# Optimization experiments

Measured on AMD Instinct MI355X. Metric: run time of the kernel, lower is better.

Reference implementation:

```python
import jax, jax.numpy as jnp
import numpy as np

B, S, D, H, O = 32, 2048, 512, 512, 512


def setup_inputs() -> dict:
    key = jax.random.key(0)
    ks = jax.random.split(key, 10)
    def w(k, shape, fan_in):
        return (jax.random.uniform(k, shape, dtype=jnp.float32) * 2.0 - 1.0) / np.float32(np.sqrt(fan_in))
    return {
        "x": jax.random.normal(ks[0], (B, S, D), dtype=jnp.float32),
        "timespans": jax.random.uniform(ks[1], (B, S, 1), dtype=jnp.float32),
        "Wx_lstm": w(ks[2], (D, 4 * H), D),
        "Wh_lstm": w(ks[3], (H, 4 * H), H),
        "b_lstm": jnp.zeros((4 * H,), dtype=jnp.float32),
        "Wx_ode": w(ks[4], (D, H), D),
        "Wh_ode": w(ks[5], (H, H), H),
        "b_ode": jnp.zeros((H,), dtype=jnp.float32),
        "Wfc": w(ks[6], (H, O), H),
        "bfc": jnp.zeros((O,), dtype=jnp.float32),
    }


def reference(x, timespans, Wx_lstm, Wh_lstm, b_lstm, Wx_ode, Wh_ode, b_ode, Wfc, bfc):
    b, s, d = x.shape
    h_dim = Wh_ode.shape[0]
    # Precompute input projections for all timesteps (hoisted out of the scan).
    xz_lstm = jnp.einsum('bsd,dk->bsk', x, Wx_lstm) + b_lstm   # (B,S,4H)
    xz_ode = jnp.einsum('bsd,dh->bsh', x, Wx_ode) + b_ode      # (B,S,H)
    ts = timespans[..., 0]                                      # (B,S), matches ts.squeeze()

    def step(carry, inp):
        h, c = carry
        zl, zo, t = inp                      # (B,4H), (B,H), (B,)
        # LSTM memory update (mixed-memory part)
        z = zl + h @ Wh_lstm
        i, f, g, o = jnp.split(z, 4, axis=-1)
        c_new = jax.nn.sigmoid(f) * c + jax.nn.sigmoid(i) * jnp.tanh(g)
        h_mem = jax.nn.sigmoid(o) * jnp.tanh(c_new)
        # Heun (RK2) ODE step: dh/dt = tanh(Wx x + Wh h + b)
        def f_ode(hh):
            return jnp.tanh(zo + hh @ Wh_ode)
        tcol = t[:, None]
        k1 = f_ode(h_mem)
        k2 = f_ode(h_mem + tcol * k1)
        h_new = h_mem + 0.5 * tcol * (k1 + k2)
        return (h_new, c_new), h_new

    carry0 = (jnp.zeros((b, h_dim), x.dtype), jnp.zeros((b, h_dim), x.dtype))
    xs = (jnp.swapaxes(xz_lstm, 0, 1), jnp.swapaxes(xz_ode, 0, 1), ts.T)
    (h_last, c_last), hs = jax.lax.scan(step, carry0, xs)       # hs: (S,B,H)
    outputs = jnp.einsum('sbh,ho->sbo', hs, Wfc) + bfc
    outputs = jnp.swapaxes(outputs, 0, 1)                       # (B,S,O)
    return outputs, h_last, c_last
```

## Files before the change

kernel.cpp:

```cpp
#include <hip/hip_runtime.h>

typedef unsigned short u16;
typedef unsigned int u32;
typedef unsigned long long u64;
typedef __attribute__((ext_vector_type(4))) float f32x4;
typedef __attribute__((ext_vector_type(8))) short bf16x8;
typedef __attribute__((ext_vector_type(4))) u16 u16x4;
typedef __attribute__((ext_vector_type(8))) u16 u16x8;
typedef __attribute__((ext_vector_type(4))) u32 u32x4;

#define AGENT_SCOPE __HIP_MEMORY_SCOPE_AGENT

__device__ __forceinline__ u64 lda64(const u64* p) {
  return __hip_atomic_load((u64*)p, __ATOMIC_RELAXED, AGENT_SCOPE);
}
__device__ __forceinline__ int loadai(const int* p) {
  return __hip_atomic_load((int*)p, __ATOMIC_RELAXED, AGENT_SCOPE);
}
__device__ __forceinline__ void sta32(u32* p, u32 v) {
  __hip_atomic_store(p, v, __ATOMIC_RELAXED, AGENT_SCOPE);
}

__device__ __forceinline__ u16 f2bf(float f) {
  u32 u = __builtin_bit_cast(u32, f);
  u = (u + 0x7FFFu + ((u >> 16) & 1u)) >> 16;
  return (u16)u;
}
__device__ __forceinline__ float b2f(u16 h) {
  return __builtin_bit_cast(float, ((u32)h) << 16);
}
__device__ __forceinline__ float sigf(float x) { return 1.0f / (1.0f + __expf(-x)); }
__device__ __forceinline__ float tanh_(float x) { return 2.0f / (1.0f + __expf(-2.0f * x)) - 1.0f; }

__global__ __launch_bounds__(256) void cvt_bf16_vec(
    const float* __restrict__ in, u16* __restrict__ out, int n4)
{
  int i = blockIdx.x * blockDim.x + threadIdx.x;
  const int stride = gridDim.x * blockDim.x;
  for (; i < n4; i += stride) {
    f32x4 v = ((const f32x4*)in)[i];
    u16x4 o;
    #pragma unroll
    for (int e = 0; e < 4; ++e) o[e] = f2bf(v[e]);
    ((u16x4*)out)[i] = o;
  }
}

__global__ __launch_bounds__(256) void transpose_f32_bf16(
    const float* __restrict__ in, u16* __restrict__ out, int R, int C)
{
  __shared__ float t[32][33];
  const int tx = threadIdx.x & 31, ty = threadIdx.x >> 5;
  const int bx = blockIdx.x * 32, by = blockIdx.y * 32;
  #pragma unroll
  for (int i = 0; i < 4; ++i)
    t[ty + i * 8][tx] = in[(long)(by + ty + i * 8) * C + bx + tx];
  __syncthreads();
  #pragma unroll
  for (int i = 0; i < 4; ++i)
    out[(long)(bx + ty + i * 8) * R + by + tx] = f2bf(t[tx][ty + i * 8]);
}

template <bool BF16_OUT>
__global__ __launch_bounds__(256, 2) void gemm_bt(
    const u16* __restrict__ A, const u16* __restrict__ Bt,
    const float* __restrict__ bias, void* __restrict__ Cv,
    int M, int N, int K)
{
  __shared__ u16 As[128 * 64];
  __shared__ u16 Bs[128 * 64];
  const int tid = threadIdx.x;
  const int lane = tid & 63;
  const int wv = tid >> 6;
  const int wm = wv >> 1, wn = wv & 1;
  const long row0 = (long)blockIdx.x * 128;
  const long col0 = (long)blockIdx.y * 128;
  const int lr8 = lane >> 3, lc8 = lane & 7;
  const int fr = lane & 15, fk = (lane >> 4) * 8;
  f32x4 acc[4][4] = {};

  for (int kt = 0; kt < K; kt += 64) {
    __syncthreads();
    #pragma unroll
    for (int ch = 0; ch < 4; ++ch) {
      const int r = wv * 32 + ch * 8;
      const u16* gA = A + (row0 + r + lr8) * (long)K + kt + lc8 * 8;
      __builtin_amdgcn_global_load_lds(
          (const __attribute__((address_space(1))) u32*)gA,
          (__attribute__((address_space(3))) u32*)&As[r * 64], 16, 0, 0);
      const u16* gB = Bt + (col0 + r + lr8) * (long)K + kt + lc8 * 8;
      __builtin_amdgcn_global_load_lds(
          (const __attribute__((address_space(1))) u32*)gB,
          (__attribute__((address_space(3))) u32*)&Bs[r * 64], 16, 0, 0);
    }
    __syncthreads();
    #pragma unroll
    for (int kk = 0; kk < 2; ++kk) {
      bf16x8 af[4], bfv[4];
      #pragma unroll
      for (int m = 0; m < 4; ++m)
        af[m] = *(const bf16x8*)&As[(wm * 64 + m * 16 + fr) * 64 + kk * 32 + fk];
      #pragma unroll
      for (int n = 0; n < 4; ++n)
        bfv[n] = *(const bf16x8*)&Bs[(wn * 64 + n * 16 + fr) * 64 + kk * 32 + fk];
      #pragma unroll
      for (int m = 0; m < 4; ++m)
        #pragma unroll
        for (int n = 0; n < 4; ++n)
          acc[m][n] = __builtin_amdgcn_mfma_f32_16x16x32_bf16(af[m], bfv[n], acc[m][n], 0, 0, 0);
    }
  }

  const int orow = (lane >> 4) * 4, ocol = lane & 15;
  #pragma unroll
  for (int m = 0; m < 4; ++m) {
    #pragma unroll
    for (int n = 0; n < 4; ++n) {
      const long cb = col0 + wn * 64 + n * 16 + ocol;
      const float bv = bias[cb];
      #pragma unroll
      for (int r = 0; r < 4; ++r) {
        const long rr = row0 + wm * 64 + m * 16 + orow + r;
        const float v = acc[m][n][r] + bv;
        if (BF16_OUT) ((u16*)Cv)[rr * (long)N + cb] = f2bf(v);
        else          ((float*)Cv)[rr * (long)N + cb] = v;
      }
    }
  }
}

#define SS 2048
#define FAROFF 16384

__device__ __forceinline__ bool ge4(u32x4 v, u32 t) {
  return ((v[0] >> 16) >= t) & ((v[1] >> 16) >= t) &
         ((v[2] >> 16) >= t) & ((v[3] >> 16) >= t);
}
__device__ __forceinline__ bool ge2(u64 w, u32 t) {
  return ((((u32)(w >> 16)) & 0xffffu) >= t) & (((u32)(w >> 48)) >= t);
}

__device__ __forceinline__ void ld8_sc0(const u32* p, u32x4& a, u32x4& b) {
  asm volatile("global_load_dwordx4 %0, %2, off sc0\n\t"
               "global_load_dwordx4 %1, %3, off sc0\n\t"
               "s_waitcnt vmcnt(0)"
               : "=&v"(a), "=&v"(b) : "v"(p), "v"(p + 4));
}
__device__ __forceinline__ void ld8_sc1(const u32* p, u32x4& a, u32x4& b) {
  asm volatile("global_load_dwordx4 %0, %2, off sc1\n\t"
               "global_load_dwordx4 %1, %3, off sc1\n\t"
               "s_waitcnt vmcnt(0)"
               : "=&v"(a), "=&v"(b) : "v"(p), "v"(p + 4));
}

__device__ __forceinline__ void pollfar(const u32* pf, u32 tag, u32x4& a, u32x4& b) {
  const u64* q = (const u64*)pf;
  u64 w0 = lda64(q), w1 = lda64(q + 1), w2 = lda64(q + 2), w3 = lda64(q + 3);
  int tries = 0;
  while (!(ge2(w0, tag) & ge2(w1, tag) & ge2(w2, tag) & ge2(w3, tag))) {
    if (++tries > 2) __builtin_amdgcn_s_sleep(1);
    w0 = lda64(q); w1 = lda64(q + 1); w2 = lda64(q + 2); w3 = lda64(q + 3);
  }
  a[0] = (u32)w0; a[1] = (u32)(w0 >> 32); a[2] = (u32)w1; a[3] = (u32)(w1 >> 32);
  b[0] = (u32)w2; b[1] = (u32)(w2 >> 32); b[2] = (u32)w3; b[3] = (u32)(w3 >> 32);
}

__device__ __forceinline__ void poll8(const u32* pn, u32 tag, int lvl, int* lvlsh,
                                      u32x4& a, u32x4& b) {
  if (lvl == 0) {
    int tries = 0;
    for (;;) {
      ld8_sc0(pn, a, b);
      if (ge4(a, tag) && ge4(b, tag)) return;
      if (++tries > 8000) { *lvlsh = 1; lvl = 1; break; }
      if (tries > 32) __builtin_amdgcn_s_sleep(1);
    }
  }
  if (lvl == 1) {
    int tries = 0;
    for (;;) {
      ld8_sc1(pn, a, b);
      if (ge4(a, tag) && ge4(b, tag)) return;
      if (++tries > 8000) { *lvlsh = 2; break; }
      if (tries > 32) __builtin_amdgcn_s_sleep(1);
    }
  }
  pollfar(pn + FAROFF, tag, a, b);
}

__device__ __forceinline__ void stdual(u32* pn, u32 word, bool far_grp) {
  sta32(pn + FAROFF, word);
  if (!far_grp)
    asm volatile("global_store_dword %0, %1, off sc1" :: "v"(pn), "v"(word) : "memory");
}

__global__ __launch_bounds__(256, 1) void scan_kernel(
    const u16* __restrict__ XZL, const float* __restrict__ XZO,
    const float* __restrict__ TS,
    const u16* __restrict__ WhlT, const u16* __restrict__ WhoT,
    u32* Ht, u32* HMt, u32* Ut,
    u16* __restrict__ HS,
    float* __restrict__ out_h, float* __restrict__ out_c,
    int* chk)
{
  const int tid = threadIdx.x;
  const int lane = tid & 63;
  const int wv = tid >> 6;
  const int fr = lane & 15;
  const int hi = lane >> 4;

  __shared__ u16 whl_l[4][16][512];
  __shared__ u16 who_l[16][512];
  __shared__ u16 stage_l[4][512];
  __shared__ u16 xcl[256];
  __shared__ int lvl_sh;

  if (tid == 0) {
    u32 xcc;
    asm volatile("s_getreg_b32 %0, hwreg(HW_REG_XCC_ID)" : "=s"(xcc));
    sta32((u32*)&chk[blockIdx.x], (xcc & 7u) + 1u);
    lvl_sh = 0;
  }
  {
    int v;
    do { v = loadai(&chk[tid]); } while (v == 0);
    xcl[tid] = (u16)(v - 1);
  }
  __syncthreads();

  int g, w;
  bool far_grp;
  {
    int cnt[8] = {0, 0, 0, 0, 0, 0, 0, 0};
    const int my = (int)xcl[blockIdx.x];
    int rank = 0;
    for (int bi = 0; bi < 256; ++bi) {
      const int e = (int)xcl[bi];
      ++cnt[e];
      rank += (e == my && bi < (int)blockIdx.x) ? 1 : 0;
    }
    bool ok = true;
    #pragma unroll
    for (int e = 0; e < 8; ++e) ok = ok && (cnt[e] == 32);
    if (ok) { g = my; w = rank; far_grp = false; }
    else    { g = (int)(blockIdx.x & 7); w = (int)(blockIdx.x >> 3); far_grp = true; }
  }
  const int j0 = w * 16;
  const int b = g * 4 + wv;

  {
    const int g4 = wv;
    #pragma unroll
    for (int ks = 0; ks < 16; ++ks)
      *(u16x8*)&whl_l[g4][ks][lane * 8] =
        *(const u16x8*)&WhlT[(size_t)(g4 * 512 + j0 + fr) * 512 + ks * 32 + hi * 8];
    for (int ks = wv; ks < 16; ks += 4)
      *(u16x8*)&who_l[ks][lane * 8] =
        *(const u16x8*)&WhoT[(size_t)(j0 + fr) * 512 + ks * 32 + hi * 8];
  }
  __syncthreads();

  u32* const Hb  = Ht  + g * 2048 + wv * 512;
  u32* const HMb = HMt + g * 2048 + wv * 512;
  u32* const Ub  = Ut  + g * 2048 + wv * 512;

  float zb_c[4], zo_c, t_c;
  {
    const u16* p = XZL + ((size_t)b * SS + 0) * 2048 + j0 + fr;
    zb_c[0] = b2f(p[0]); zb_c[1] = b2f(p[512]);
    zb_c[2] = b2f(p[1024]); zb_c[3] = b2f(p[1536]);
    zo_c = XZO[((size_t)b * SS + 0) * 512 + j0 + fr];
    t_c  = TS[(size_t)b * SS + 0];
  }

  float c_r = 0.0f;
  u32x4 pa, pb;

  for (int s = 0; s < SS; ++s) {
    const u32 tagv = (u32)(s + 1);
    int lvl = far_grp ? 2 : *(volatile int*)&lvl_sh;

    if (s == 0) {
      u16x8 z8 = {0, 0, 0, 0, 0, 0, 0, 0};
      *(u16x8*)&stage_l[wv][lane * 8] = z8;
    } else {
      poll8(Hb + lane * 8, (u32)s, lvl, &lvl_sh, pa, pb);
      u16x8 hv;
      #pragma unroll
      for (int i = 0; i < 4; ++i) {
        hv[i] = (u16)(pa[i] & 0xffffu);
        hv[4 + i] = (u16)(pb[i] & 0xffffu);
      }
      *(u16x8*)&stage_l[wv][lane * 8] = hv;
    }

    f32x4 az0 = {}, az1 = {}, az2 = {}, az3 = {};
    #pragma unroll
    for (int ks = 0; ks < 16; ++ks) {
      bf16x8 af = *(const bf16x8*)&stage_l[wv][ks * 32 + hi * 8];
      az0 = __builtin_amdgcn_mfma_f32_16x16x32_bf16(af, *(const bf16x8*)&whl_l[0][ks][lane * 8], az0, 0, 0, 0);
      az1 = __builtin_amdgcn_mfma_f32_16x16x32_bf16(af, *(const bf16x8*)&whl_l[1][ks][lane * 8], az1, 0, 0, 0);
      az2 = __builtin_amdgcn_mfma_f32_16x16x32_bf16(af, *(const bf16x8*)&whl_l[2][ks][lane * 8], az2, 0, 0, 0);
      az3 = __builtin_amdgcn_mfma_f32_16x16x32_bf16(af, *(const bf16x8*)&whl_l[3][ks][lane * 8], az3, 0, 0, 0);
    }

    const float zi = az0[0] + zb_c[0];
    const float zf = az1[0] + zb_c[1];
    const float zg = az2[0] + zb_c[2];
    const float zo = az3[0] + zb_c[3];
    const float cn = sigf(zf) * c_r + sigf(zi) * tanh_(zg);
    const float hm = sigf(zo) * tanh_(cn);
    c_r = cn;
    if (hi == 0) stdual(&HMb[j0 + fr], (tagv << 16) | (u32)f2bf(hm), far_grp);

    const int sn = (s + 1 < SS) ? s + 1 : s;
    float zb_n[4], zo_n, t_n;
    {
      const u16* p = XZL + ((size_t)b * SS + sn) * 2048 + j0 + fr;
      zb_n[0] = b2f(p[0]); zb_n[1] = b2f(p[512]);
      zb_n[2] = b2f(p[1024]); zb_n[3] = b2f(p[1536]);
      zo_n = XZO[((size_t)b * SS + sn) * 512 + j0 + fr];
      t_n  = TS[(size_t)b * SS + sn];
    }

    lvl = far_grp ? 2 : *(volatile int*)&lvl_sh;
    poll8(HMb + lane * 8, tagv, lvl, &lvl_sh, pa, pb);
    {
      u16x8 hv;
      #pragma unroll
      for (int i = 0; i < 4; ++i) {
        hv[i] = (u16)(pa[i] & 0xffffu);
        hv[4 + i] = (u16)(pb[i] & 0xffffu);
      }
      *(u16x8*)&stage_l[wv][lane * 8] = hv;
    }
    f32x4 ak = {};
    #pragma unroll
    for (int ks = 0; ks < 16; ++ks) {
      bf16x8 af = *(const bf16x8*)&stage_l[wv][ks * 32 + hi * 8];
      ak = __builtin_amdgcn_mfma_f32_16x16x32_bf16(af, *(const bf16x8*)&who_l[ks][lane * 8], ak, 0, 0, 0);
    }
    const float k1 = tanh_(zo_c + ak[0]);
    const float uu = hm + t_c * k1;
    if (hi == 0) stdual(&Ub[j0 + fr], (tagv << 16) | (u32)f2bf(uu), far_grp);

    lvl = far_grp ? 2 : *(volatile int*)&lvl_sh;
    poll8(Ub + lane * 8, tagv, lvl, &lvl_sh, pa, pb);
    {
      u16x8 hv;
      #pragma unroll
      for (int i = 0; i < 4; ++i) {
        hv[i] = (u16)(pa[i] & 0xffffu);
        hv[4 + i] = (u16)(pb[i] & 0xffffu);
      }
      *(u16x8*)&stage_l[wv][lane * 8] = hv;
    }
    f32x4 ak2 = {};
    #pragma unroll
    for (int ks = 0; ks < 16; ++ks) {
      bf16x8 af = *(const bf16x8*)&stage_l[wv][ks * 32 + hi * 8];
      ak2 = __builtin_amdgcn_mfma_f32_16x16x32_bf16(af, *(const bf16x8*)&who_l[ks][lane * 8], ak2, 0, 0, 0);
    }
    const float k2 = tanh_(zo_c + ak2[0]);
    const float hn = hm + 0.5f * t_c * (k1 + k2);
    if (hi == 0) {
      stdual(&Hb[j0 + fr], (tagv << 16) | (u32)f2bf(hn), far_grp);
      HS[((size_t)b * SS + s) * 512 + j0 + fr] = f2bf(hn);
      if (s == SS - 1) out_h[(size_t)b * 512 + j0 + fr] = hn;
    }

    #pragma unroll
    for (int i = 0; i < 4; ++i) zb_c[i] = zb_n[i];
    zo_c = zo_n; t_c = t_n;
  }

  if (hi == 0) out_c[(size_t)b * 512 + j0 + fr] = c_r;
}

extern "C" void kernel_launch(void* const* d_in, const int* in_sizes, int n_in,
                              void* d_out, int out_size, void* d_ws, size_t ws_size,
                              hipStream_t stream)
{
  const long B = 32, S = 2048, O = 512;
  const long MS = B * S;

  const float* x   = (const float*)d_in[0];
  const float* ts  = (const float*)d_in[1];
  const float* Wxl = (const float*)d_in[2];
  const float* Whl = (const float*)d_in[3];
  const float* bl  = (const float*)d_in[4];
  const float* Wxo = (const float*)d_in[5];
  const float* Who = (const float*)d_in[6];
  const float* bo  = (const float*)d_in[7];
  const float* Wfc = (const float*)d_in[8];
  const float* bfc = (const float*)d_in[9];

  float* out = (float*)d_out;
  float* out_h = out + MS * O;
  float* out_c = out_h + B * 512;

  char* ws = (char*)d_ws;
  size_t off = 0;
  auto alloc = [&](size_t bytes) -> void* {
    void* p = ws + off;
    off += (bytes + 255) & ~(size_t)255;
    return p;
  };
  u16*   XZL  = (u16*)  alloc(MS * 2048 * 2);
  u16*   xb   = (u16*)  alloc(MS * 512 * 2);
  u16*   HS   = xb;
  u16*   WxlT = (u16*)  alloc(2048 * 512 * 2);
  u16*   WhlT = (u16*)  alloc(2048 * 512 * 2);
  u16*   WxoT = (u16*)  alloc(512 * 512 * 2);
  u16*   WhoT = (u16*)  alloc(512 * 512 * 2);
  u16*   WfcT = (u16*)  alloc(512 * 512 * 2);
  u32*   Ht   = (u32*)  alloc(2 * 8 * 2048 * 4);
  u32*   HMt  = (u32*)  alloc(2 * 8 * 2048 * 4);
  u32*   Ut   = (u32*)  alloc(2 * 8 * 2048 * 4);
  int*   chk  = (int*)  alloc(1024);

  float* XZO = out;

  if (off > ws_size) return;

  hipMemsetAsync(Ht, 0, 2 * 8 * 2048 * 4, stream);
  hipMemsetAsync(HMt, 0, 2 * 8 * 2048 * 4, stream);
  hipMemsetAsync(Ut, 0, 2 * 8 * 2048 * 4, stream);
  hipMemsetAsync(chk, 0, 1024, stream);

  cvt_bf16_vec<<<2048, 256, 0, stream>>>(x, xb, (int)(MS * 512 / 4));
  transpose_f32_bf16<<<dim3(64, 16), 256, 0, stream>>>(Wxl, WxlT, 512, 2048);
  transpose_f32_bf16<<<dim3(64, 16), 256, 0, stream>>>(Whl, WhlT, 512, 2048);
  transpose_f32_bf16<<<dim3(16, 16), 256, 0, stream>>>(Wxo, WxoT, 512, 512);
  transpose_f32_bf16<<<dim3(16, 16), 256, 0, stream>>>(Who, WhoT, 512, 512);
  transpose_f32_bf16<<<dim3(16, 16), 256, 0, stream>>>(Wfc, WfcT, 512, 512);

  gemm_bt<true ><<<dim3(512, 16), 256, 0, stream>>>(xb, WxlT, bl, XZL, (int)MS, 2048, 512);
  gemm_bt<false><<<dim3(512, 4), 256, 0, stream>>>(xb, WxoT, bo, XZO, (int)MS, 512, 512);

  {
    void* args[] = { (void*)&XZL, (void*)&XZO, (void*)&ts, (void*)&WhlT, (void*)&WhoT,
                     (void*)&Ht, (void*)&HMt, (void*)&Ut, (void*)&HS,
                     (void*)&out_h, (void*)&out_c, (void*)&chk };
    hipLaunchCooperativeKernel((void*)scan_kernel, dim3(256), dim3(256), args, 0, stream);
  }

  gemm_bt<false><<<dim3(512, 4), 256, 0, stream>>>(HS, WfcT, bfc, out, (int)MS, 512, 512);
}
```

Measured before the change: 12.45 ms.

## Defer far-path flag stores and HS writes off the critical path; split MFMA chains

Each flag store to the far (cross-XCD) mirror is now deferred until after the local sc1 store and the following poll, unless the block is already polling at the far level. The HS history write for step s is moved into step s+1 after the poll, and the final h is written after the loop. Each MFMA accumulation chain is split into two independent halves to shorten dependency latency. The aim is to get the near-path flags published sooner and cut serial MFMA latency per step. The cost is delayed visibility of far flags, which could slow blocks that wait on them.

```diff
diff --git a/kernel.cpp b/kernel.cpp
--- a/kernel.cpp
+++ b/kernel.cpp
@@ -188,12 +188,6 @@
   pollfar(pn + FAROFF, tag, a, b);
 }
 
-__device__ __forceinline__ void stdual(u32* pn, u32 word, bool far_grp) {
-  sta32(pn + FAROFF, word);
-  if (!far_grp)
-    asm volatile("global_store_dword %0, %1, off sc1" :: "v"(pn), "v"(word) : "memory");
-}
-
 __global__ __launch_bounds__(256, 1) void scan_kernel(
     const u16* __restrict__ XZL, const float* __restrict__ XZO,
     const float* __restrict__ TS,
@@ -253,13 +247,14 @@
     #pragma unroll
     for (int ks = 0; ks < 16; ++ks)
       *(u16x8*)&whl_l[g4][ks][lane * 8] =
-        *(const u16x8*)&WhlT[(size_t)(g4 * 512 + j0 + fr) * 512 + ks * 32 + hi * 8];
+        *(const u16x8*)&WhlT[(size_t)(g4 * 512 + j0 + fr) * 512 + ks * 32 + (lane >> 4) * 8];
     for (int ks = wv; ks < 16; ks += 4)
       *(u16x8*)&who_l[ks][lane * 8] =
-        *(const u16x8*)&WhoT[(size_t)(j0 + fr) * 512 + ks * 32 + hi * 8];
+        *(const u16x8*)&WhoT[(size_t)(j0 + fr) * 512 + ks * 32 + (lane >> 4) * 8];
   }
   __syncthreads();
 
+  const int kc8 = hi * 8;
   u32* const Hb  = Ht  + g * 2048 + wv * 512;
   u32* const HMb = HMt + g * 2048 + wv * 512;
   u32* const Ub  = Ut  + g * 2048 + wv * 512;
@@ -275,6 +270,9 @@
 
   float c_r = 0.0f;
   u32x4 pa, pb;
+  u32* pend_p = nullptr;
+  u32  pend_w = 0;
+  float hn_pend = 0.0f;
 
   for (int s = 0; s < SS; ++s) {
     const u32 tagv = (u32)(s + 1);
@@ -284,6 +282,7 @@
       u16x8 z8 = {0, 0, 0, 0, 0, 0, 0, 0};
       *(u16x8*)&stage_l[wv][lane * 8] = z8;
     } else {
+      if (hi == 0 && lvl >= 2 && pend_p) { sta32(pend_p, pend_w); pend_p = nullptr; }
       poll8(Hb + lane * 8, (u32)s, lvl, &lvl_sh, pa, pb);
       u16x8 hv;
       #pragma unroll
@@ -292,26 +291,45 @@
         hv[4 + i] = (u16)(pb[i] & 0xffffu);
       }
       *(u16x8*)&stage_l[wv][lane * 8] = hv;
-    }
-
-    f32x4 az0 = {}, az1 = {}, az2 = {}, az3 = {};
-    #pragma unroll
-    for (int ks = 0; ks < 16; ++ks) {
-      bf16x8 af = *(const bf16x8*)&stage_l[wv][ks * 32 + hi * 8];
-      az0 = __builtin_amdgcn_mfma_f32_16x16x32_bf16(af, *(const bf16x8*)&whl_l[0][ks][lane * 8], az0, 0, 0, 0);
-      az1 = __builtin_amdgcn_mfma_f32_16x16x32_bf16(af, *(const bf16x8*)&whl_l[1][ks][lane * 8], az1, 0, 0, 0);
-      az2 = __builtin_amdgcn_mfma_f32_16x16x32_bf16(af, *(const bf16x8*)&whl_l[2][ks][lane * 8], az2, 0, 0, 0);
-      az3 = __builtin_amdgcn_mfma_f32_16x16x32_bf16(af, *(const bf16x8*)&whl_l[3][ks][lane * 8], az3, 0, 0, 0);
-    }
-
-    const float zi = az0[0] + zb_c[0];
-    const float zf = az1[0] + zb_c[1];
-    const float zg = az2[0] + zb_c[2];
-    const float zo = az3[0] + zb_c[3];
+      if (hi == 0) {
+        if (pend_p) { sta32(pend_p, pend_w); pend_p = nullptr; }
+        HS[((size_t)b * SS + (s - 1)) * 512 + j0 + fr] = f2bf(hn_pend);
+      }
+    }
+
+    f32x4 az0a = {}, az0b = {}, az1a = {}, az1b = {};
+    f32x4 az2a = {}, az2b = {}, az3a = {}, az3b = {};
+    #pragma unroll
+    for (int ks = 0; ks < 8; ++ks) {
+      bf16x8 afa = *(const bf16x8*)&stage_l[wv][ks * 32 + kc8];
+      bf16x8 afb = *(const bf16x8*)&stage_l[wv][(ks + 8) * 32 + kc8];
+      az0a = __builtin_amdgcn_mfma_f32_16x16x32_bf16(afa, *(const bf16x8*)&whl_l[0][ks][lane * 8], az0a, 0, 0, 0);
+      az0b = __builtin_amdgcn_mfma_f32_16x16x32_bf16(afb, *(const bf16x8*)&whl_l[0][ks + 8][lane * 8], az0b, 0, 0, 0);
+      az1a = __builtin_amdgcn_mfma_f32_16x16x32_bf16(afa, *(const bf16x8*)&whl_l[1][ks][lane * 8], az1a, 0, 0, 0);
+      az1b = __builtin_amdgcn_mfma_f32_16x16x32_bf16(afb, *(const bf16x8*)&whl_l[1][ks + 8][lane * 8], az1b, 0, 0, 0);
+      az2a = __builtin_amdgcn_mfma_f32_16x16x32_bf16(afa, *(const bf16x8*)&whl_l[2][ks][lane * 8], az2a, 0, 0, 0);
+      az2b = __builtin_amdgcn_mfma_f32_16x16x32_bf16(afb, *(const bf16x8*)&whl_l[2][ks + 8][lane * 8], az2b, 0, 0, 0);
+      az3a = __builtin_amdgcn_mfma_f32_16x16x32_bf16(afa, *(const bf16x8*)&whl_l[3][ks][lane * 8], az3a, 0, 0, 0);
+      az3b = __builtin_amdgcn_mfma_f32_16x16x32_bf16(afb, *(const bf16x8*)&whl_l[3][ks + 8][lane * 8], az3b, 0, 0, 0);
+    }
+
+    const float zi = az0a[0] + az0b[0] + zb_c[0];
+    const float zf = az1a[0] + az1b[0] + zb_c[1];
+    const float zg = az2a[0] + az2b[0] + zb_c[2];
+    const float zo = az3a[0] + az3b[0] + zb_c[3];
     const float cn = sigf(zf) * c_r + sigf(zi) * tanh_(zg);
     const float hm = sigf(zo) * tanh_(cn);
     c_r = cn;
-    if (hi == 0) stdual(&HMb[j0 + fr], (tagv << 16) | (u32)f2bf(hm), far_grp);
+    if (hi == 0) {
+      const u32 wd = (tagv << 16) | (u32)f2bf(hm);
+      if (!far_grp)
+        asm volatile("global_store_dword %0, %1, off sc1" :: "v"(&HMb[j0 + fr]), "v"(wd) : "memory");
+      pend_p = &HMb[j0 + fr] + FAROFF; pend_w = wd;
+    }
+
+    lvl = far_grp ? 2 : *(volatile int*)&lvl_sh;
+    if (hi == 0 && lvl >= 2 && pend_p) { sta32(pend_p, pend_w); pend_p = nullptr; }
+    poll8(HMb + lane * 8, tagv, lvl, &lvl_sh, pa, pb);
 
     const int sn = (s + 1 < SS) ? s + 1 : s;
     float zb_n[4], zo_n, t_n;
@@ -322,9 +340,7 @@
       zo_n = XZO[((size_t)b * SS + sn) * 512 + j0 + fr];
       t_n  = TS[(size_t)b * SS + sn];
     }
-
-    lvl = far_grp ? 2 : *(volatile int*)&lvl_sh;
-    poll8(HMb + lane * 8, tagv, lvl, &lvl_sh, pa, pb);
+    if (hi == 0 && pend_p) { sta32(pend_p, pend_w); pend_p = nullptr; }
     {
       u16x8 hv;
       #pragma unroll
@@ -334,18 +350,27 @@
       }
       *(u16x8*)&stage_l[wv][lane * 8] = hv;
     }
-    f32x4 ak = {};
-    #pragma unroll
-    for (int ks = 0; ks < 16; ++ks) {
-      bf16x8 af = *(const bf16x8*)&stage_l[wv][ks * 32 + hi * 8];
-      ak = __builtin_amdgcn_mfma_f32_16x16x32_bf16(af, *(const bf16x8*)&who_l[ks][lane * 8], ak, 0, 0, 0);
-    }
-    const float k1 = tanh_(zo_c + ak[0]);
+    f32x4 aka = {}, akb = {};
+    #pragma unroll
+    for (int ks = 0; ks < 8; ++ks) {
+      bf16x8 afa = *(const bf16x8*)&stage_l[wv][ks * 32 + kc8];
+      bf16x8 afb = *(const bf16x8*)&stage_l[wv][(ks + 8) * 32 + kc8];
+      aka = __builtin_amdgcn_mfma_f32_16x16x32_bf16(afa, *(const bf16x8*)&who_l[ks][lane * 8], aka, 0, 0, 0);
+      akb = __builtin_amdgcn_mfma_f32_16x16x32_bf16(afb, *(const bf16x8*)&who_l[ks + 8][lane * 8], akb, 0, 0, 0);
+    }
+    const float k1 = tanh_(zo_c + aka[0] + akb[0]);
     const float uu = hm + t_c * k1;
-    if (hi == 0) stdual(&Ub[j0 + fr], (tagv << 16) | (u32)f2bf(uu), far_grp);
+    if (hi == 0) {
+      const u32 wd = (tagv << 16) | (u32)f2bf(uu);
+      if (!far_grp)
+        asm volatile("global_store_dword %0, %1, off sc1" :: "v"(&Ub[j0 + fr]), "v"(wd) : "memory");
+      pend_p = &Ub[j0 + fr] + FAROFF; pend_w = wd;
+    }
 
     lvl = far_grp ? 2 : *(volatile int*)&lvl_sh;
+    if (hi == 0 && lvl >= 2 && pend_p) { sta32(pend_p, pend_w); pend_p = nullptr; }
     poll8(Ub + lane * 8, tagv, lvl, &lvl_sh, pa, pb);
+    if (hi == 0 && pend_p) { sta32(pend_p, pend_w); pend_p = nullptr; }
     {
       u16x8 hv;
       #pragma unroll
@@ -355,18 +380,22 @@
       }
       *(u16x8*)&stage_l[wv][lane * 8] = hv;
     }
-    f32x4 ak2 = {};
-    #pragma unroll
-    for (int ks = 0; ks < 16; ++ks) {
-      bf16x8 af = *(const bf16x8*)&stage_l[wv][ks * 32 + hi * 8];
-      ak2 = __builtin_amdgcn_mfma_f32_16x16x32_bf16(af, *(const bf16x8*)&who_l[ks][lane * 8], ak2, 0, 0, 0);
-    }
-    const float k2 = tanh_(zo_c + ak2[0]);
+    f32x4 a2a = {}, a2b = {};
+    #pragma unroll
+    for (int ks = 0; ks < 8; ++ks) {
+      bf16x8 afa = *(const bf16x8*)&stage_l[wv][ks * 32 + kc8];
+      bf16x8 afb = *(const bf16x8*)&stage_l[wv][(ks + 8) * 32 + kc8];
+      a2a = __builtin_amdgcn_mfma_f32_16x16x32_bf16(afa, *(const bf16x8*)&who_l[ks][lane * 8], a2a, 0, 0, 0);
+      a2b = __builtin_amdgcn_mfma_f32_16x16x32_bf16(afb, *(const bf16x8*)&who_l[ks + 8][lane * 8], a2b, 0, 0, 0);
+    }
+    const float k2 = tanh_(zo_c + a2a[0] + a2b[0]);
     const float hn = hm + 0.5f * t_c * (k1 + k2);
     if (hi == 0) {
-      stdual(&Hb[j0 + fr], (tagv << 16) | (u32)f2bf(hn), far_grp);
-      HS[((size_t)b * SS + s) * 512 + j0 + fr] = f2bf(hn);
-      if (s == SS - 1) out_h[(size_t)b * 512 + j0 + fr] = hn;
+      const u32 wd = (tagv << 16) | (u32)f2bf(hn);
+      if (!far_grp)
+        asm volatile("global_store_dword %0, %1, off sc1" :: "v"(&Hb[j0 + fr]), "v"(wd) : "memory");
+      pend_p = &Hb[j0 + fr] + FAROFF; pend_w = wd;
+      hn_pend = hn;
     }
 
     #pragma unroll
@@ -374,7 +403,12 @@
     zo_c = zo_n; t_c = t_n;
   }
 
-  if (hi == 0) out_c[(size_t)b * 512 + j0 + fr] = c_r;
+  if (hi == 0) {
+    if (pend_p) sta32(pend_p, pend_w);
+    HS[((size_t)b * SS + (SS - 1)) * 512 + j0 + fr] = f2bf(hn_pend);
+    out_h[(size_t)b * 512 + j0 + fr] = hn_pend;
+    out_c[(size_t)b * 512 + j0 + fr] = c_r;
+  }
 }
 
 extern "C" void kernel_launch(void* const* d_in, const int* in_sizes, int n_in,
```

Measured after the change: 13.77 ms (median of 2 runs). +10.6%, slower.
